# Optimization experiments

Measured on AMD Instinct MI355X. Metric: run time of the kernel, lower is better.

## Reference

```python
import jax, jax.numpy as jnp
import numpy as np

DIM = 512
HEADS = 8
HEAD_DIM = DIM // HEADS
SCALE = HEAD_DIM ** -0.5


def setup_inputs() -> dict:
    key = jax.random.key(0)
    ks = jax.random.split(key, 7)
    B, QN, N = 32, 128, 4096
    q = jax.random.normal(ks[0], (B, QN, DIM), dtype=jnp.float32)
    kv = jax.random.normal(ks[1], (B, N, DIM), dtype=jnp.float32)
    key_mask = jax.random.normal(ks[2], (B, QN, N), dtype=jnp.float32)
    Wq = jax.random.normal(ks[3], (DIM, DIM), dtype=jnp.float32) * 0.02
    Wkv = jax.random.normal(ks[4], (2 * DIM, DIM), dtype=jnp.float32) * 0.02
    Wproj = jax.random.normal(ks[5], (DIM, DIM), dtype=jnp.float32) * 0.02
    bproj = jax.random.normal(ks[6], (DIM,), dtype=jnp.float32) * 0.02
    return {"q": q, "kv": kv, "key_mask": key_mask,
            "Wq": Wq, "Wkv": Wkv, "Wproj": Wproj, "bproj": bproj}


def reference(q, kv, key_mask, Wq, Wkv, Wproj, bproj):
    B, QN, C = q.shape
    N = kv.shape[1]
    # q projection -> [B, QN, H, hd]
    qh = (q @ Wq.T).reshape(B, QN, HEADS, HEAD_DIM) * SCALE
    # kv projection -> split into k, v each [B, N, H, hd]
    kvp = kv @ Wkv.T  # [B, N, 2C]
    k = kvp[..., :C].reshape(B, N, HEADS, HEAD_DIM)
    v = kvp[..., C:].reshape(B, N, HEADS, HEAD_DIM)
    # scores [B, H, QN, N] + additive mask broadcast over heads
    attn = jnp.einsum('bqhd,bkhd->bhqk', qh, k) + key_mask[:, None]
    attn = jax.nn.softmax(attn, axis=-1)
    x = jnp.einsum('bhqk,bkhd->bqhd', attn, v).reshape(B, QN, C)
    return x @ Wproj.T + bproj
```

## Files before the change

kernel.cpp:

```cpp
#include <hip/hip_runtime.h>
#include <hip/hip_bf16.h>

typedef __attribute__((ext_vector_type(4))) float f32x4;
typedef __attribute__((ext_vector_type(8))) short bf16x8;

#define GAS __attribute__((address_space(1)))
#define LAS __attribute__((address_space(3)))

__device__ __forceinline__ unsigned int cvtpk(float lo, float hi) {
  unsigned int r;
  asm("v_cvt_pk_bf16_f32 %0, %1, %2" : "=v"(r) : "v"(lo), "v"(hi));
  return r;
}
__device__ __forceinline__ unsigned short f2bf(float f) { return (unsigned short)cvtpk(f, f); }
__device__ __forceinline__ f32x4 mfma16(bf16x8 a, bf16x8 b, f32x4 c) {
  return __builtin_amdgcn_mfma_f32_16x16x32_bf16(a, b, c, 0, 0, 0);
}
__device__ __forceinline__ void gl_lds16(const unsigned short* g, unsigned short* l) {
  __builtin_amdgcn_global_load_lds((const GAS unsigned short*)g, (LAS unsigned short*)l, 16, 0, 0);
}
__device__ __forceinline__ void memfence_sched() { asm volatile("" ::: "memory"); }

__global__ __launch_bounds__(256)
void cvt_f32_bf16(const float* __restrict__ in, unsigned short* __restrict__ out, int n8) {
  for (int i = blockIdx.x * blockDim.x + threadIdx.x; i < n8; i += gridDim.x * blockDim.x) {
    const float4 a = *reinterpret_cast<const float4*>(in + (size_t)i * 8);
    const float4 b = *reinterpret_cast<const float4*>(in + (size_t)i * 8 + 4);
    uint4 o;
    o.x = cvtpk(a.x, a.y); o.y = cvtpk(a.z, a.w);
    o.z = cvtpk(b.x, b.y); o.w = cvtpk(b.z, b.w);
    *reinterpret_cast<uint4*>(out + (size_t)i * 8) = o;
  }
}

template<int MODE, bool AF32, bool BF32>
__global__ __launch_bounds__(512, 2)
void gemm8(const void* __restrict__ Agv, const void* __restrict__ Bgv,
           void* __restrict__ Cg, const float* __restrict__ bias, int ntn, size_t ldc)
{
  constexpr int NA = AF32 ? 2 : 3;
  constexpr int NB = BF32 ? 2 : 3;
  constexpr int SOPS = (AF32 || BF32) ? 6 : 4;
  __shared__ unsigned short sm[(NA + NB) * 8192];
  unsigned short* const smB = sm + NA * 8192;

  const int t = threadIdx.x, lane = t & 63, w = t >> 6;
  const int lo = lane & 15, hi = lane >> 4;
  const int wm = w >> 2, wn = w & 3;
  const int nwg = gridDim.x, bid = blockIdx.x;
  const int id = (bid & 7) * (nwg >> 3) + (bid >> 3);
  const int row0 = (id / ntn) * 256, col0 = (id % ntn) * 256;
  const int w16 = w * 16;

  const unsigned short* Ab = (const unsigned short*)Agv;
  const unsigned short* Bb = (const unsigned short*)Bgv;
  const float* Af = (const float*)Agv;
  const float* Bf = (const float*)Bgv;

  const int cxor_g = (lane >> 3) & 3;
  const size_t a_src_g = (size_t)(row0 + w16 + (lane >> 2)) * 512 + (((lane & 3) ^ cxor_g) << 3);
  const size_t b_src_g = (size_t)(col0 + w16 + (lane >> 2)) * 512 + (((lane & 3) ^ cxor_g) << 3);

  const int rs_r = t >> 2;
  const int rs_c = (t & 3) * 8;
  const int wch = ((t & 3) ^ ((t >> 3) & 3)) << 3;

  float4 stA[2][4];
  float4 stB[2][4];

  auto A_ISSUE = [&](int kt, int bank) {
    if constexpr (AF32) {
      const float* s0 = Af + (size_t)(row0 + rs_r) * 512 + kt * 32 + rs_c;
      const float* s1 = Af + (size_t)(row0 + 128 + rs_r) * 512 + kt * 32 + rs_c;
      stA[bank][0] = *(const float4*)s0; stA[bank][1] = *(const float4*)(s0 + 4);
      stA[bank][2] = *(const float4*)s1; stA[bank][3] = *(const float4*)(s1 + 4);
    } else {
      unsigned short* ab = &sm[(kt % NA) * 8192];
      gl_lds16(Ab + a_src_g + kt * 32, ab + w16 * 32);
      gl_lds16(Ab + a_src_g + (size_t)128 * 512 + kt * 32, ab + (128 + w16) * 32);
    }
  };
  auto B_ISSUE = [&](int kt, int bank) {
    if constexpr (BF32) {
      const float* s0 = Bf + (size_t)(col0 + rs_r) * 512 + kt * 32 + rs_c;
      const float* s1 = Bf + (size_t)(col0 + 128 + rs_r) * 512 + kt * 32 + rs_c;
      stB[bank][0] = *(const float4*)s0; stB[bank][1] = *(const float4*)(s0 + 4);
      stB[bank][2] = *(const float4*)s1; stB[bank][3] = *(const float4*)(s1 + 4);
    } else {
      unsigned short* bb = &smB[(kt % NB) * 8192];
      gl_lds16(Bb + b_src_g + kt * 32, bb + w16 * 32);
      gl_lds16(Bb + b_src_g + (size_t)128 * 512 + kt * 32, bb + (128 + w16) * 32);
    }
  };
  auto A_WRITE = [&](int kt, int bank) {
    if constexpr (AF32) {
      unsigned short* ab = &sm[(kt % NA) * 8192];
      uint4 o;
      o.x = cvtpk(stA[bank][0].x, stA[bank][0].y); o.y = cvtpk(stA[bank][0].z, stA[bank][0].w);
      o.z = cvtpk(stA[bank][1].x, stA[bank][1].y); o.w = cvtpk(stA[bank][1].z, stA[bank][1].w);
      *reinterpret_cast<uint4*>(&ab[rs_r * 32 + wch]) = o;
      o.x = cvtpk(stA[bank][2].x, stA[bank][2].y); o.y = cvtpk(stA[bank][2].z, stA[bank][2].w);
      o.z = cvtpk(stA[bank][3].x, stA[bank][3].y); o.w = cvtpk(stA[bank][3].z, stA[bank][3].w);
      *reinterpret_cast<uint4*>(&ab[(128 + rs_r) * 32 + wch]) = o;
    }
  };
  auto B_WRITE = [&](int kt, int bank) {
    if constexpr (BF32) {
      unsigned short* bb = &smB[(kt % NB) * 8192];
      uint4 o;
      o.x = cvtpk(stB[bank][0].x, stB[bank][0].y); o.y = cvtpk(stB[bank][0].z, stB[bank][0].w);
      o.z = cvtpk(stB[bank][1].x, stB[bank][1].y); o.w = cvtpk(stB[bank][1].z, stB[bank][1].w);
      *reinterpret_cast<uint4*>(&bb[rs_r * 32 + wch]) = o;
      o.x = cvtpk(stB[bank][2].x, stB[bank][2].y); o.y = cvtpk(stB[bank][2].z, stB[bank][2].w);
      o.z = cvtpk(stB[bank][3].x, stB[bank][3].y); o.w = cvtpk(stB[bank][3].z, stB[bank][3].w);
      *reinterpret_cast<uint4*>(&bb[(128 + rs_r) * 32 + wch]) = o;
    }
  };

  f32x4 acc[8][4] = {};
  const int fxor = (hi ^ ((lo >> 1) & 3)) << 3;

  A_ISSUE(0, 0); B_ISSUE(0, 0);
  A_ISSUE(1, 1); B_ISSUE(1, 1);
  memfence_sched();
  if constexpr (SOPS == 6) asm volatile("s_waitcnt vmcnt(6)" ::: "memory");
  else                     asm volatile("s_waitcnt vmcnt(4)" ::: "memory");
  A_WRITE(0, 0); B_WRITE(0, 0);
  asm volatile("s_waitcnt lgkmcnt(0)" ::: "memory");
  __builtin_amdgcn_s_barrier();
  memfence_sched();

  #pragma unroll
  for (int kt = 0; kt < 16; ++kt) {
    const unsigned short* ab = &sm[(kt % NA) * 8192];
    const unsigned short* bb = &smB[(kt % NB) * 8192];
    bf16x8 bfr[4], af[4];
    #pragma unroll
    for (int nj = 0; nj < 4; ++nj)
      bfr[nj] = *reinterpret_cast<const bf16x8*>(&bb[(wn * 64 + nj * 16 + lo) * 32 + fxor]);
    #pragma unroll
    for (int mi = 0; mi < 4; ++mi)
      af[mi] = *reinterpret_cast<const bf16x8*>(&ab[(wm * 128 + mi * 16 + lo) * 32 + fxor]);
    if (kt + 2 <= 15) { A_ISSUE(kt + 2, kt & 1); B_ISSUE(kt + 2, kt & 1); }
    memfence_sched();
    __builtin_amdgcn_s_setprio(1);
    #pragma unroll
    for (int mi = 0; mi < 4; ++mi)
      #pragma unroll
      for (int nj = 0; nj < 4; ++nj)
        acc[mi][nj] = mfma16(af[mi], bfr[nj], acc[mi][nj]);
    __builtin_amdgcn_s_setprio(0);
    #pragma unroll
    for (int mi = 0; mi < 4; ++mi)
      af[mi] = *reinterpret_cast<const bf16x8*>(&ab[(wm * 128 + (mi + 4) * 16 + lo) * 32 + fxor]);
    if (kt <= 14) {
      if (kt + 2 <= 15) {
        if constexpr (SOPS == 6) asm volatile("s_waitcnt vmcnt(6)" ::: "memory");
        else                     asm volatile("s_waitcnt vmcnt(4)" ::: "memory");
      } else {
        asm volatile("s_waitcnt vmcnt(0)" ::: "memory");
      }
      A_WRITE(kt + 1, (kt + 1) & 1); B_WRITE(kt + 1, (kt + 1) & 1);
    }
    __builtin_amdgcn_s_setprio(1);
    #pragma unroll
    for (int mi = 0; mi < 4; ++mi)
      #pragma unroll
      for (int nj = 0; nj < 4; ++nj)
        acc[mi + 4][nj] = mfma16(af[mi], bfr[nj], acc[mi + 4][nj]);
    __builtin_amdgcn_s_setprio(0);
    if (kt < 15) {
      asm volatile("s_waitcnt lgkmcnt(0)" ::: "memory");
      __builtin_amdgcn_s_barrier();
      memfence_sched();
    }
  }

  #pragma unroll
  for (int mi = 0; mi < 8; ++mi) {
    #pragma unroll
    for (int r = 0; r < 4; ++r) {
      const size_t gm = (size_t)row0 + wm * 128 + mi * 16 + hi * 4 + r;
      #pragma unroll
      for (int nj = 0; nj < 4; ++nj) {
        const int gn = col0 + wn * 64 + nj * 16 + lo;
        const float v = acc[mi][nj][r];
        if constexpr (MODE == 0)
          ((unsigned short*)Cg)[gm * ldc + gn] = f2bf(v * 0.125f);
        else if constexpr (MODE == 1)
          ((unsigned short*)Cg)[gm * ldc + gn] = f2bf(v);
        else
          ((float*)Cg)[gm * ldc + gn] = v + bias[gn];
      }
    }
  }
}

__global__ __launch_bounds__(256)
void attn_fwd(const unsigned short* __restrict__ qh,
              const unsigned short* __restrict__ kbuf,
              const unsigned short* __restrict__ vT,
              const float* __restrict__ mask,
              float* __restrict__ opart, float* __restrict__ ml)
{
  __shared__ unsigned short Ks[64 * 64];
  __shared__ unsigned short Vs[64 * 64];
  __shared__ unsigned short Ps[4][16 * 64];
  const int bid = blockIdx.x;
  const int xcd = bid & 7, g = bid >> 3;
  const int b = (g >> 6) * 8 + xcd;
  const int sub = g & 63;
  const int h = sub >> 3, qhalf = (sub >> 2) & 1, c = sub & 3;
  const int n0 = c * 1024;
  const int bh2 = (b * 8 + h) * 2 + qhalf;
  const int t = threadIdx.x, lane = t & 63, w = t >> 6;
  const int hi = lane >> 4, lo = lane & 15;
  const int q0 = qhalf * 64 + w * 16;

  bf16x8 aq[2];
  #pragma unroll
  for (int kk = 0; kk < 2; ++kk)
    aq[kk] = *reinterpret_cast<const bf16x8*>(
        qh + (size_t)(b * 128 + q0 + lo) * 512 + h * 64 + kk * 32 + hi * 8);

  float mrow[4], lrow[4];
  #pragma unroll
  for (int i = 0; i < 4; ++i) { mrow[i] = -1e30f; lrow[i] = 0.f; }
  f32x4 o[4] = {};

  const unsigned short* kp = kbuf + ((size_t)b * 4096 + n0) * 512 + h * 64;
  const unsigned short* vp = vT + (size_t)(h * 64) * 131072 + (size_t)b * 4096 + n0;
  const float* mp = mask + ((size_t)(b * 128 + q0)) * 4096 + n0;

  for (int nt = 0; nt < 16; ++nt) {
    {
      const int r = t >> 3, cc = t & 7;
      *reinterpret_cast<uint4*>(&Ks[r * 64 + ((cc ^ (r & 7)) << 3)]) =
          *reinterpret_cast<const uint4*>(kp + (size_t)(nt * 64 + r) * 512 + (cc << 3));
      *reinterpret_cast<uint4*>(&Ks[(r + 32) * 64 + ((cc ^ (r & 7)) << 3)]) =
          *reinterpret_cast<const uint4*>(kp + (size_t)(nt * 64 + r + 32) * 512 + (cc << 3));
      *reinterpret_cast<uint4*>(&Vs[r * 64 + ((cc ^ (r & 7)) << 3)]) =
          *reinterpret_cast<const uint4*>(vp + (size_t)r * 131072 + nt * 64 + (cc << 3));
      *reinterpret_cast<uint4*>(&Vs[(r + 32) * 64 + ((cc ^ (r & 7)) << 3)]) =
          *reinterpret_cast<const uint4*>(vp + (size_t)(r + 32) * 131072 + nt * 64 + (cc << 3));
    }
    __syncthreads();

    f32x4 s[4] = {};
    __builtin_amdgcn_s_setprio(1);
    #pragma unroll
    for (int ni = 0; ni < 4; ++ni) {
      #pragma unroll
      for (int kk = 0; kk < 2; ++kk) {
        const bf16x8 kf = *reinterpret_cast<const bf16x8*>(
            &Ks[(ni * 16 + lo) * 64 + ((kk * 32 + hi * 8) ^ ((lo & 7) << 3))]);
        s[ni] = mfma16(aq[kk], kf, s[ni]);
      }
    }
    __builtin_amdgcn_s_setprio(0);
    #pragma unroll
    for (int ni = 0; ni < 4; ++ni)
      #pragma unroll
      for (int r = 0; r < 4; ++r)
        s[ni][r] += mp[(size_t)(hi * 4 + r) * 4096 + nt * 64 + ni * 16 + lo];

    #pragma unroll
    for (int r = 0; r < 4; ++r) {
      float mx = fmaxf(fmaxf(s[0][r], s[1][r]), fmaxf(s[2][r], s[3][r]));
      #pragma unroll
      for (int off = 1; off < 16; off <<= 1)
        mx = fmaxf(mx, __shfl_xor(mx, off, 64));
      const float mnew = fmaxf(mrow[r], mx);
      const float corr = __expf(mrow[r] - mnew);
      mrow[r] = mnew;
      float ls = 0.f;
      #pragma unroll
      for (int ni = 0; ni < 4; ++ni) {
        const float p = __expf(s[ni][r] - mnew);
        s[ni][r] = p; ls += p;
      }
      #pragma unroll
      for (int off = 1; off < 16; off <<= 1)
        ls += __shfl_xor(ls, off, 64);
      lrow[r] = lrow[r] * corr + ls;
      #pragma unroll
      for (int di = 0; di < 4; ++di)
        o[di][r] *= corr;
    }

    #pragma unroll
    for (int ni = 0; ni < 4; ++ni)
      #pragma unroll
      for (int r = 0; r < 4; ++r) {
        const int rp = hi * 4 + r;
        Ps[w][rp * 64 + ((ni * 16 + lo) ^ ((rp & 7) << 3))] = f2bf(s[ni][r]);
      }

    __builtin_amdgcn_s_setprio(1);
    #pragma unroll
    for (int kk = 0; kk < 2; ++kk) {
      const bf16x8 pa = *reinterpret_cast<const bf16x8*>(
          &Ps[w][lo * 64 + ((kk * 32 + hi * 8) ^ ((lo & 7) << 3))]);
      #pragma unroll
      for (int di = 0; di < 4; ++di) {
        const bf16x8 vf = *reinterpret_cast<const bf16x8*>(
            &Vs[(di * 16 + lo) * 64 + ((kk * 32 + hi * 8) ^ ((lo & 7) << 3))]);
        o[di] = mfma16(pa, vf, o[di]);
      }
    }
    __builtin_amdgcn_s_setprio(0);
    __syncthreads();
  }

  const size_t pbase = ((size_t)bh2 * 4 + c) * 64;
  #pragma unroll
  for (int di = 0; di < 4; ++di)
    #pragma unroll
    for (int r = 0; r < 4; ++r)
      opart[(pbase + (w * 16 + hi * 4 + r)) * 64 + di * 16 + lo] = o[di][r];
  if (lo == 0) {
    #pragma unroll
    for (int r = 0; r < 4; ++r) {
      const int qq = w * 16 + hi * 4 + r;
      ml[(((size_t)bh2 * 4 + c) * 2 + 0) * 64 + qq] = mrow[r];
      ml[(((size_t)bh2 * 4 + c) * 2 + 1) * 64 + qq] = lrow[r];
    }
  }
}

__global__ __launch_bounds__(256)
void attn_combine(const float* __restrict__ opart, const float* __restrict__ ml,
                  unsigned short* __restrict__ xb)
{
  const int bh2 = blockIdx.x;
  const int b = bh2 >> 4, h = (bh2 >> 1) & 7, qhalf = bh2 & 1;
  const int t = threadIdx.x;
  const int q = t >> 2, dg = t & 3;

  float m[4], l[4];
  #pragma unroll
  for (int c = 0; c < 4; ++c) {
    m[c] = ml[(((size_t)bh2 * 4 + c) * 2 + 0) * 64 + q];
    l[c] = ml[(((size_t)bh2 * 4 + c) * 2 + 1) * 64 + q];
  }
  const float M = fmaxf(fmaxf(m[0], m[1]), fmaxf(m[2], m[3]));
  float sc[4], L = 0.f;
  #pragma unroll
  for (int c = 0; c < 4; ++c) { sc[c] = __expf(m[c] - M); L += sc[c] * l[c]; }
  const float inv = 1.f / L;

  float4 acc[4] = {};
  #pragma unroll
  for (int c = 0; c < 4; ++c) {
    const float* base = opart + (((size_t)bh2 * 4 + c) * 64 + q) * 64 + dg * 16;
    #pragma unroll
    for (int j = 0; j < 4; ++j) {
      const float4 v = *reinterpret_cast<const float4*>(base + j * 4);
      acc[j].x = fmaf(sc[c], v.x, acc[j].x);
      acc[j].y = fmaf(sc[c], v.y, acc[j].y);
      acc[j].z = fmaf(sc[c], v.z, acc[j].z);
      acc[j].w = fmaf(sc[c], v.w, acc[j].w);
    }
  }
  unsigned short* dst = xb + ((size_t)b * 128 + qhalf * 64 + q) * 512 + h * 64 + dg * 16;
  uint4 o1, o2;
  o1.x = cvtpk(acc[0].x * inv, acc[0].y * inv); o1.y = cvtpk(acc[0].z * inv, acc[0].w * inv);
  o1.z = cvtpk(acc[1].x * inv, acc[1].y * inv); o1.w = cvtpk(acc[1].z * inv, acc[1].w * inv);
  o2.x = cvtpk(acc[2].x * inv, acc[2].y * inv); o2.y = cvtpk(acc[2].z * inv, acc[2].w * inv);
  o2.z = cvtpk(acc[3].x * inv, acc[3].y * inv); o2.w = cvtpk(acc[3].z * inv, acc[3].w * inv);
  *reinterpret_cast<uint4*>(dst) = o1;
  *reinterpret_cast<uint4*>(dst + 8) = o2;
}

extern "C" void kernel_launch(void* const* d_in, const int* in_sizes, int n_in,
                              void* d_out, int out_size, void* d_ws, size_t ws_size,
                              hipStream_t stream) {
  const float* q     = (const float*)d_in[0];
  const float* kv    = (const float*)d_in[1];
  const float* mask  = (const float*)d_in[2];
  const float* Wq    = (const float*)d_in[3];
  const float* Wkv   = (const float*)d_in[4];
  const float* Wproj = (const float*)d_in[5];
  const float* bproj = (const float*)d_in[6];
  float* out = (float*)d_out;

  char* ws = (char*)d_ws;
  unsigned short* kbuf   = (unsigned short*)ws;
  unsigned short* vTb    = (unsigned short*)(ws + 134217728ULL);
  float*          opart  = (float*)(ws + 268435456ULL);
  float*          mlb    = (float*)(ws + 301989888ULL);
  unsigned short* qhb    = (unsigned short*)(ws + 303038464ULL);
  unsigned short* xb     = (unsigned short*)(ws + 307232768ULL);
  unsigned short* Wqb    = (unsigned short*)(ws + 311427072ULL);
  unsigned short* Wkvb   = (unsigned short*)(ws + 311951360ULL);
  unsigned short* Wprojb = (unsigned short*)(ws + 312999936ULL);

  cvt_f32_bf16<<<128, 256, 0, stream>>>(Wq, Wqb, 512 * 512 / 8);
  cvt_f32_bf16<<<256, 256, 0, stream>>>(Wkv, Wkvb, 1024 * 512 / 8);
  cvt_f32_bf16<<<128, 256, 0, stream>>>(Wproj, Wprojb, 512 * 512 / 8);

  gemm8<0, true, false><<<32, 512, 0, stream>>>(q, Wqb, qhb, nullptr, 2, 512);
  gemm8<1, true, false><<<1024, 512, 0, stream>>>(kv, Wkvb, kbuf, nullptr, 2, 512);
  gemm8<1, false, true><<<1024, 512, 0, stream>>>(Wkvb + 512 * 512, kv, vTb, nullptr, 512, 131072);
  attn_fwd<<<2048, 256, 0, stream>>>(qhb, kbuf, vTb, mask, opart, mlb);
  attn_combine<<<512, 256, 0, stream>>>(opart, mlb, xb);
  gemm8<2, false, false><<<32, 512, 0, stream>>>(xb, Wprojb, out, bproj, 2, 512);
}
```

Measured before the change: 449.2 us.

## Deepen fp32 operand prefetch to three stages with explicit vmcnt accounting

Restructures the mixed fp32/bf16 GEMM pipeline so the fp32 operand is prefetched three k-tiles ahead into a triple register bank, while the bf16 operand stays on direct-to-LDS loads two tiles ahead. Waits are rewritten as per-iteration vmcnt counts that track the interleaved load streams, and the barrier wait for direct LDS loads is now placed explicitly before each barrier. The aim is to hide global-load latency for the fp32 side of the projection GEMMs. It costs extra registers for the third bank, and the hand-tuned vmcnt values must exactly match the issue order.

```diff
diff --git a/kernel.cpp b/kernel.cpp
--- a/kernel.cpp
+++ b/kernel.cpp
@@ -38,9 +38,9 @@
 void gemm8(const void* __restrict__ Agv, const void* __restrict__ Bgv,
            void* __restrict__ Cg, const float* __restrict__ bias, int ntn, size_t ldc)
 {
+  constexpr bool MIXED = AF32 || BF32;
   constexpr int NA = AF32 ? 2 : 3;
   constexpr int NB = BF32 ? 2 : 3;
-  constexpr int SOPS = (AF32 || BF32) ? 6 : 4;
   __shared__ unsigned short sm[(NA + NB) * 8192];
   unsigned short* const smB = sm + NA * 8192;
 
@@ -54,8 +54,8 @@
 
   const unsigned short* Ab = (const unsigned short*)Agv;
   const unsigned short* Bb = (const unsigned short*)Bgv;
-  const float* Af = (const float*)Agv;
-  const float* Bf = (const float*)Bgv;
+  const float* Ff = AF32 ? (const float*)Agv : (const float*)Bgv;
+  const int frow0 = AF32 ? row0 : col0;
 
   const int cxor_g = (lane >> 3) & 3;
   const size_t a_src_g = (size_t)(row0 + w16 + (lane >> 2)) * 512 + (((lane & 3) ^ cxor_g) << 3);
@@ -65,67 +65,59 @@
   const int rs_c = (t & 3) * 8;
   const int wch = ((t & 3) ^ ((t >> 3) & 3)) << 3;
 
-  float4 stA[2][4];
-  float4 stB[2][4];
-
-  auto A_ISSUE = [&](int kt, int bank) {
-    if constexpr (AF32) {
-      const float* s0 = Af + (size_t)(row0 + rs_r) * 512 + kt * 32 + rs_c;
-      const float* s1 = Af + (size_t)(row0 + 128 + rs_r) * 512 + kt * 32 + rs_c;
-      stA[bank][0] = *(const float4*)s0; stA[bank][1] = *(const float4*)(s0 + 4);
-      stA[bank][2] = *(const float4*)s1; stA[bank][3] = *(const float4*)(s1 + 4);
-    } else {
+  float4 stF[3][4];
+
+  auto F_ISSUE = [&](int kt) {
+    if constexpr (MIXED) {
+      const int bk = kt % 3;
+      const float* s0 = Ff + (size_t)(frow0 + rs_r) * 512 + kt * 32 + rs_c;
+      const float* s1 = Ff + (size_t)(frow0 + 128 + rs_r) * 512 + kt * 32 + rs_c;
+      stF[bk][0] = *(const float4*)s0; stF[bk][1] = *(const float4*)(s0 + 4);
+      stF[bk][2] = *(const float4*)s1; stF[bk][3] = *(const float4*)(s1 + 4);
+    }
+  };
+  auto F_WRITE = [&](int kt) {
+    if constexpr (MIXED) {
+      const int bk = kt % 3;
+      unsigned short* fb = AF32 ? &sm[(kt % NA) * 8192] : &smB[(kt % NB) * 8192];
+      uint4 o;
+      o.x = cvtpk(stF[bk][0].x, stF[bk][0].y); o.y = cvtpk(stF[bk][0].z, stF[bk][0].w);
+      o.z = cvtpk(stF[bk][1].x, stF[bk][1].y); o.w = cvtpk(stF[bk][1].z, stF[bk][1].w);
+      *reinterpret_cast<uint4*>(&fb[rs_r * 32 + wch]) = o;
+      o.x = cvtpk(stF[bk][2].x, stF[bk][2].y); o.y = cvtpk(stF[bk][2].z, stF[bk][2].w);
+      o.z = cvtpk(stF[bk][3].x, stF[bk][3].y); o.w = cvtpk(stF[bk][3].z, stF[bk][3].w);
+      *reinterpret_cast<uint4*>(&fb[(128 + rs_r) * 32 + wch]) = o;
+    }
+  };
+  auto G_ISSUE = [&](int kt) {
+    if constexpr (!AF32) {
       unsigned short* ab = &sm[(kt % NA) * 8192];
       gl_lds16(Ab + a_src_g + kt * 32, ab + w16 * 32);
       gl_lds16(Ab + a_src_g + (size_t)128 * 512 + kt * 32, ab + (128 + w16) * 32);
     }
-  };
-  auto B_ISSUE = [&](int kt, int bank) {
-    if constexpr (BF32) {
-      const float* s0 = Bf + (size_t)(col0 + rs_r) * 512 + kt * 32 + rs_c;
-      const float* s1 = Bf + (size_t)(col0 + 128 + rs_r) * 512 + kt * 32 + rs_c;
-      stB[bank][0] = *(const float4*)s0; stB[bank][1] = *(const float4*)(s0 + 4);
-      stB[bank][2] = *(const float4*)s1; stB[bank][3] = *(const float4*)(s1 + 4);
-    } else {
+    if constexpr (!BF32) {
       unsigned short* bb = &smB[(kt % NB) * 8192];
       gl_lds16(Bb + b_src_g + kt * 32, bb + w16 * 32);
       gl_lds16(Bb + b_src_g + (size_t)128 * 512 + kt * 32, bb + (128 + w16) * 32);
     }
   };
-  auto A_WRITE = [&](int kt, int bank) {
-    if constexpr (AF32) {
-      unsigned short* ab = &sm[(kt % NA) * 8192];
-      uint4 o;
-      o.x = cvtpk(stA[bank][0].x, stA[bank][0].y); o.y = cvtpk(stA[bank][0].z, stA[bank][0].w);
-      o.z = cvtpk(stA[bank][1].x, stA[bank][1].y); o.w = cvtpk(stA[bank][1].z, stA[bank][1].w);
-      *reinterpret_cast<uint4*>(&ab[rs_r * 32 + wch]) = o;
-      o.x = cvtpk(stA[bank][2].x, stA[bank][2].y); o.y = cvtpk(stA[bank][2].z, stA[bank][2].w);
-      o.z = cvtpk(stA[bank][3].x, stA[bank][3].y); o.w = cvtpk(stA[bank][3].z, stA[bank][3].w);
-      *reinterpret_cast<uint4*>(&ab[(128 + rs_r) * 32 + wch]) = o;
-    }
-  };
-  auto B_WRITE = [&](int kt, int bank) {
-    if constexpr (BF32) {
-      unsigned short* bb = &smB[(kt % NB) * 8192];
-      uint4 o;
-      o.x = cvtpk(stB[bank][0].x, stB[bank][0].y); o.y = cvtpk(stB[bank][0].z, stB[bank][0].w);
-      o.z = cvtpk(stB[bank][1].x, stB[bank][1].y); o.w = cvtpk(stB[bank][1].z, stB[bank][1].w);
-      *reinterpret_cast<uint4*>(&bb[rs_r * 32 + wch]) = o;
-      o.x = cvtpk(stB[bank][2].x, stB[bank][2].y); o.y = cvtpk(stB[bank][2].z, stB[bank][2].w);
-      o.z = cvtpk(stB[bank][3].x, stB[bank][3].y); o.w = cvtpk(stB[bank][3].z, stB[bank][3].w);
-      *reinterpret_cast<uint4*>(&bb[(128 + rs_r) * 32 + wch]) = o;
-    }
-  };
 
   f32x4 acc[8][4] = {};
   const int fxor = (hi ^ ((lo >> 1) & 3)) << 3;
 
-  A_ISSUE(0, 0); B_ISSUE(0, 0);
-  A_ISSUE(1, 1); B_ISSUE(1, 1);
-  memfence_sched();
-  if constexpr (SOPS == 6) asm volatile("s_waitcnt vmcnt(6)" ::: "memory");
-  else                     asm volatile("s_waitcnt vmcnt(4)" ::: "memory");
-  A_WRITE(0, 0); B_WRITE(0, 0);
+  if constexpr (MIXED) {
+    F_ISSUE(0);
+    G_ISSUE(0); F_ISSUE(1);
+    G_ISSUE(1); F_ISSUE(2);
+    memfence_sched();
+    asm volatile("s_waitcnt vmcnt(12)" ::: "memory");
+    F_WRITE(0);
+    asm volatile("s_waitcnt vmcnt(10)" ::: "memory");
+  } else {
+    G_ISSUE(0); G_ISSUE(1);
+    memfence_sched();
+    asm volatile("s_waitcnt vmcnt(4)" ::: "memory");
+  }
   asm volatile("s_waitcnt lgkmcnt(0)" ::: "memory");
   __builtin_amdgcn_s_barrier();
   memfence_sched();
@@ -141,8 +133,15 @@
     #pragma unroll
     for (int mi = 0; mi < 4; ++mi)
       af[mi] = *reinterpret_cast<const bf16x8*>(&ab[(wm * 128 + mi * 16 + lo) * 32 + fxor]);
-    if (kt + 2 <= 15) { A_ISSUE(kt + 2, kt & 1); B_ISSUE(kt + 2, kt & 1); }
+
+    if constexpr (MIXED) {
+      if (kt <= 13) G_ISSUE(kt + 2);
+      if (kt <= 12) F_ISSUE(kt + 3);
+    } else {
+      if (kt <= 13) G_ISSUE(kt + 2);
+    }
     memfence_sched();
+
     __builtin_amdgcn_s_setprio(1);
     #pragma unroll
     for (int mi = 0; mi < 4; ++mi)
@@ -150,18 +149,18 @@
       for (int nj = 0; nj < 4; ++nj)
         acc[mi][nj] = mfma16(af[mi], bfr[nj], acc[mi][nj]);
     __builtin_amdgcn_s_setprio(0);
+
     #pragma unroll
     for (int mi = 0; mi < 4; ++mi)
       af[mi] = *reinterpret_cast<const bf16x8*>(&ab[(wm * 128 + (mi + 4) * 16 + lo) * 32 + fxor]);
-    if (kt <= 14) {
-      if (kt + 2 <= 15) {
-        if constexpr (SOPS == 6) asm volatile("s_waitcnt vmcnt(6)" ::: "memory");
-        else                     asm volatile("s_waitcnt vmcnt(4)" ::: "memory");
-      } else {
-        asm volatile("s_waitcnt vmcnt(0)" ::: "memory");
-      }
-      A_WRITE(kt + 1, (kt + 1) & 1); B_WRITE(kt + 1, (kt + 1) & 1);
-    }
+
+    if constexpr (MIXED) {
+      if (kt <= 12)      { asm volatile("s_waitcnt vmcnt(12)" ::: "memory"); }
+      else if (kt == 13) { asm volatile("s_waitcnt vmcnt(8)"  ::: "memory"); }
+      else if (kt == 14) { asm volatile("s_waitcnt vmcnt(2)"  ::: "memory"); }
+      if (kt <= 14) F_WRITE(kt + 1);
+    }
+
     __builtin_amdgcn_s_setprio(1);
     #pragma unroll
     for (int mi = 0; mi < 4; ++mi)
@@ -169,7 +168,16 @@
       for (int nj = 0; nj < 4; ++nj)
         acc[mi + 4][nj] = mfma16(af[mi], bfr[nj], acc[mi + 4][nj]);
     __builtin_amdgcn_s_setprio(0);
+
     if (kt < 15) {
+      if constexpr (MIXED) {
+        if (kt <= 12)      { asm volatile("s_waitcnt vmcnt(10)" ::: "memory"); }
+        else if (kt == 13) { asm volatile("s_waitcnt vmcnt(6)"  ::: "memory"); }
+        else               { asm volatile("s_waitcnt vmcnt(0)"  ::: "memory"); }
+      } else {
+        if (kt <= 13)      { asm volatile("s_waitcnt vmcnt(4)" ::: "memory"); }
+        else               { asm volatile("s_waitcnt vmcnt(0)" ::: "memory"); }
+      }
       asm volatile("s_waitcnt lgkmcnt(0)" ::: "memory");
       __builtin_amdgcn_s_barrier();
       memfence_sched();
```

New measurement: 451.1 us. Within noise of the previous version (+0.4%).
